# Performance work log

Measured on AMD Instinct MI355X. Metric: run time of the kernel, lower is better.

Reference implementation:

```python
import jax, jax.numpy as jnp
import numpy as np


def setup_inputs() -> dict:
    key = jax.random.key(0)
    k1, k2 = jax.random.split(key)
    z = jax.random.normal(k1, (8, 16, 16, 16, 32), dtype=jnp.float32)
    # codebook initialized uniform(-1/K, 1/K) in the original module
    K = 8192
    emb = jax.random.uniform(k2, (K, 32), dtype=jnp.float32, minval=-1.0 / K, maxval=1.0 / K)
    return {"z": z, "emb": emb}


def reference(z, emb):
    bs, h, w, d, c = z.shape
    z_flat = z.reshape(-1, c)  # [N, c]
    # Squared Euclidean distances: ||z||^2 - 2 z.e + ||e||^2.
    # torch.cdist uses sqrt, but argmin is identical for squared distances
    # and distances are not returned, so we skip the sqrt.
    d2 = (
        jnp.sum(z_flat * z_flat, axis=-1, keepdims=True)
        - 2.0 * (z_flat @ emb.T)
        + jnp.sum(emb * emb, axis=-1)
    )  # [N, K]
    idx = jnp.argmin(d2, axis=1)  # [N]
    quantized = emb[idx].reshape(bs, h, w, d, c)
    commitment_loss = jnp.mean(jnp.square(z - jax.lax.stop_gradient(quantized)))
    vq_loss = jnp.mean(jnp.square(quantized - jax.lax.stop_gradient(z)))
    quantized_st = z + jax.lax.stop_gradient(quantized - z)  # straight-through
    return quantized_st, vq_loss, commitment_loss, idx.reshape(bs, h, w, d)
```

## Files before the change

### kernel.cpp

```cpp
#include <hip/hip_runtime.h>
#include <cfloat>
#include <stdint.h>

#define NROW   32768
#define KCODES 8192
#define CDIM   32
#define OUT_Q    0
#define OUT_LOSS 1048576
#define OUT_IDX  1048578
#define HALF_EPS 1e-4f
#define MAXCAND  32

typedef short bf8_t __attribute__((ext_vector_type(8)));
typedef float f32x4 __attribute__((ext_vector_type(4)));

__device__ __forceinline__ unsigned short f2bf(float f) {
  unsigned int u = __float_as_uint(f);
  return (unsigned short)((u + 0x7FFFu + ((u >> 16) & 1u)) >> 16);
}
__device__ __forceinline__ unsigned int xf(float f) {
  unsigned int u = __float_as_uint(f);
  return u ^ (unsigned int)(((int)u >> 31) | 0x80000000);
}
__device__ __forceinline__ float unxf(unsigned int k) {
  unsigned int u = (k & 0x80000000u) ? (k ^ 0x80000000u) : ~k;
  return __uint_as_float(u);
}

__global__ __launch_bounds__(256) void vq_prep(
    const float* __restrict__ z, const float* __restrict__ emb,
    unsigned short* __restrict__ zh, unsigned short* __restrict__ eh,
    float* __restrict__ enorm, unsigned int* __restrict__ mmax,
    int* __restrict__ ccnt, float* __restrict__ out) {
  const int t = blockIdx.x * 256 + threadIdx.x;
  {
    const float4* z4 = (const float4*)(z + (size_t)t * CDIM);
    unsigned int w[16];
#pragma unroll
    for (int j = 0; j < 8; ++j) {
      float4 v = z4[j];
      w[2 * j]     = (unsigned int)f2bf(v.x) | ((unsigned int)f2bf(v.y) << 16);
      w[2 * j + 1] = (unsigned int)f2bf(v.z) | ((unsigned int)f2bf(v.w) << 16);
    }
    uint4* o = (uint4*)(zh + (size_t)t * CDIM);
#pragma unroll
    for (int j = 0; j < 4; ++j)
      o[j] = make_uint4(w[4 * j], w[4 * j + 1], w[4 * j + 2], w[4 * j + 3]);
  }
  if (t < KCODES) {
    const float4* e4 = (const float4*)(emb + (size_t)t * CDIM);
    float s = 0.f;
    unsigned int w[16];
#pragma unroll
    for (int j = 0; j < 8; ++j) {
      float4 v = e4[j];
      s += v.x * v.x + v.y * v.y + v.z * v.z + v.w * v.w;
      w[2 * j]     = (unsigned int)f2bf(v.x) | ((unsigned int)f2bf(v.y) << 16);
      w[2 * j + 1] = (unsigned int)f2bf(v.z) | ((unsigned int)f2bf(v.w) << 16);
    }
    enorm[t] = s;
    uint4* o = (uint4*)(eh + (size_t)t * CDIM);
#pragma unroll
    for (int j = 0; j < 4; ++j)
      o[j] = make_uint4(w[4 * j], w[4 * j + 1], w[4 * j + 2], w[4 * j + 3]);
  }
  mmax[t] = 0u;
  ccnt[t] = 0;
  if (t < 2) out[OUT_LOSS + t] = 0.f;
}

__global__ __launch_bounds__(256, 4) void vq_sweep_max(
    const unsigned short* __restrict__ zh, const unsigned short* __restrict__ eh,
    unsigned int* __restrict__ mmax) {
  const int wid = threadIdx.x >> 6, lane = threadIdx.x & 63;
  const int quad = lane >> 4, col = lane & 15;
  const int rbase = blockIdx.x * 32;
  const int kbase = wid * 2048;

  bf8_t a0 = *(const bf8_t*)(zh + (size_t)(rbase + col) * CDIM + quad * 8);
  bf8_t a1 = *(const bf8_t*)(zh + (size_t)(rbase + 16 + col) * CDIM + quad * 8);

  float mx0[4], mx1[4];
#pragma unroll
  for (int i = 0; i < 4; ++i) { mx0[i] = -FLT_MAX; mx1[i] = -FLT_MAX; }

  const bf8_t* ep = (const bf8_t*)(eh + ((size_t)kbase + col) * CDIM + quad * 8);
#pragma unroll 4
  for (int t = 0; t < 128; ++t) {
    bf8_t b = ep[(size_t)t * 64];
    f32x4 d0 = __builtin_amdgcn_mfma_f32_16x16x32_bf16(
        a0, b, (f32x4){0.f, 0.f, 0.f, 0.f}, 0, 0, 0);
    f32x4 d1 = __builtin_amdgcn_mfma_f32_16x16x32_bf16(
        a1, b, (f32x4){0.f, 0.f, 0.f, 0.f}, 0, 0, 0);
#pragma unroll
    for (int i = 0; i < 4; ++i) {
      mx0[i] = fmaxf(mx0[i], d0[i]);
      mx1[i] = fmaxf(mx1[i], d1[i]);
    }
  }
#pragma unroll
  for (int off = 1; off < 16; off <<= 1) {
#pragma unroll
    for (int i = 0; i < 4; ++i) {
      mx0[i] = fmaxf(mx0[i], __shfl_xor(mx0[i], off, 64));
      mx1[i] = fmaxf(mx1[i], __shfl_xor(mx1[i], off, 64));
    }
  }
  if (col == 0) {
#pragma unroll
    for (int i = 0; i < 4; ++i) {
      atomicMax(&mmax[rbase + quad * 4 + i], xf(mx0[i]));
      atomicMax(&mmax[rbase + 16 + quad * 4 + i], xf(mx1[i]));
    }
  }
}

__global__ __launch_bounds__(256, 4) void vq_sweep_cand(
    const unsigned short* __restrict__ zh, const unsigned short* __restrict__ eh,
    const unsigned int* __restrict__ mmax, int* __restrict__ ccnt,
    int* __restrict__ cand) {
  const int wid = threadIdx.x >> 6, lane = threadIdx.x & 63;
  const int quad = lane >> 4, col = lane & 15;
  const int rbase = blockIdx.x * 32;
  const int kbase = wid * 2048;

  bf8_t a0 = *(const bf8_t*)(zh + (size_t)(rbase + col) * CDIM + quad * 8);
  bf8_t a1 = *(const bf8_t*)(zh + (size_t)(rbase + 16 + col) * CDIM + quad * 8);

  float th0[4], th1[4];
#pragma unroll
  for (int i = 0; i < 4; ++i) {
    th0[i] = unxf(mmax[rbase + quad * 4 + i]) - HALF_EPS;
    th1[i] = unxf(mmax[rbase + 16 + quad * 4 + i]) - HALF_EPS;
  }

  const bf8_t* ep = (const bf8_t*)(eh + ((size_t)kbase + col) * CDIM + quad * 8);
#pragma unroll 2
  for (int t = 0; t < 128; ++t) {
    bf8_t b = ep[(size_t)t * 64];
    f32x4 d0 = __builtin_amdgcn_mfma_f32_16x16x32_bf16(
        a0, b, (f32x4){0.f, 0.f, 0.f, 0.f}, 0, 0, 0);
    f32x4 d1 = __builtin_amdgcn_mfma_f32_16x16x32_bf16(
        a1, b, (f32x4){0.f, 0.f, 0.f, 0.f}, 0, 0, 0);
    const int code = kbase + t * 16 + col;
#pragma unroll
    for (int i = 0; i < 4; ++i) {
      if (d0[i] >= th0[i]) {
        int r = rbase + quad * 4 + i;
        int s = atomicAdd(&ccnt[r], 1);
        if (s < MAXCAND) cand[(size_t)r * MAXCAND + s] = code;
      }
      if (d1[i] >= th1[i]) {
        int r = rbase + 16 + quad * 4 + i;
        int s = atomicAdd(&ccnt[r], 1);
        if (s < MAXCAND) cand[(size_t)r * MAXCAND + s] = code;
      }
    }
  }
}

__global__ __launch_bounds__(256) void vq_final(
    const float* __restrict__ z, const float* __restrict__ emb,
    const float* __restrict__ enorm, const int* __restrict__ ccnt,
    const int* __restrict__ cand, float* __restrict__ out) {
  const int r = blockIdx.x * 256 + threadIdx.x;

  float zr[CDIM];
  const float4* z4 = (const float4*)(z + (size_t)r * CDIM);
#pragma unroll
  for (int j = 0; j < 8; ++j) {
    float4 v = z4[j];
    zr[4 * j + 0] = v.x; zr[4 * j + 1] = v.y;
    zr[4 * j + 2] = v.z; zr[4 * j + 3] = v.w;
  }
  float znorm = 0.f;
#pragma unroll
  for (int j = 0; j < CDIM; ++j) znorm = fmaf(zr[j], zr[j], znorm);

  const int n = ccnt[r];
  float best = FLT_MAX;
  int bidx = KCODES;
  if (n <= MAXCAND) {
    for (int j = 0; j < n; ++j) {
      int k = cand[(size_t)r * MAXCAND + j];
      const float* ek = emb + (size_t)k * CDIM;
      float dot = 0.f;
#pragma unroll
      for (int q = 0; q < CDIM; ++q) dot = fmaf(zr[q], ek[q], dot);
      float s = fmaf(-2.f, dot, znorm) + enorm[k];
      if (s < best || (s == best && k < bidx)) { best = s; bidx = k; }
    }
  } else {
    for (int k = 0; k < KCODES; ++k) {
      const float* ek = emb + (size_t)k * CDIM;
      float dot = 0.f;
#pragma unroll
      for (int q = 0; q < CDIM; ++q) dot = fmaf(zr[q], ek[q], dot);
      float s = fmaf(-2.f, dot, znorm) + enorm[k];
      if (s < best) { best = s; bidx = k; }
    }
  }

  const float4* q4 = (const float4*)(emb + (size_t)bidx * CDIM);
  float4* o4 = (float4*)(out + OUT_Q + (size_t)r * CDIM);
  float lsum = 0.f;
#pragma unroll
  for (int j = 0; j < 8; ++j) {
    float4 q = q4[j];
    float dx = zr[4 * j + 0] - q.x, dy = zr[4 * j + 1] - q.y;
    float dz = zr[4 * j + 2] - q.z, dw = zr[4 * j + 3] - q.w;
    lsum += dx * dx + dy * dy + dz * dz + dw * dw;
    o4[j] = q;
  }
  out[OUT_IDX + r] = (float)bidx;

#pragma unroll
  for (int off = 32; off > 0; off >>= 1) lsum += __shfl_down(lsum, off, 64);
  if ((threadIdx.x & 63) == 0) {
    float v = lsum * (1.0f / (float)(NROW * CDIM));
    atomicAdd(out + OUT_LOSS + 0, v);
    atomicAdd(out + OUT_LOSS + 1, v);
  }
}

extern "C" void kernel_launch(void* const* d_in, const int* in_sizes, int n_in,
                              void* d_out, int out_size, void* d_ws,
                              size_t ws_size, hipStream_t stream) {
  const float* z = (const float*)d_in[0];
  const float* emb = (const float*)d_in[1];
  float* out = (float*)d_out;

  float* enorm = (float*)d_ws;
  unsigned short* zh = (unsigned short*)(enorm + KCODES);
  unsigned short* eh = zh + (size_t)NROW * CDIM;
  unsigned int* mmax = (unsigned int*)(eh + (size_t)KCODES * CDIM);
  int* ccnt = (int*)(mmax + NROW);
  int* cand = ccnt + NROW;

  vq_prep<<<NROW / 256, 256, 0, stream>>>(z, emb, zh, eh, enorm, mmax, ccnt, out);
  vq_sweep_max<<<NROW / 32, 256, 0, stream>>>(zh, eh, mmax);
  vq_sweep_cand<<<NROW / 32, 256, 0, stream>>>(zh, eh, mmax, ccnt, cand);
  vq_final<<<NROW / 256, 256, 0, stream>>>(z, emb, enorm, ccnt, cand, out);
}
```

Before: 195.6 us.

## Fuse max and candidate sweeps into one block-local kernel with larger row tiles

Merges the two bf16 MFMA sweep kernels into one kernel in which each 512-thread block handles 128 rows across the whole codebook. The per-row max is reduced in shared memory instead of through global atomics, which removes the mmax buffer and one launch. Each B fragment is now reused across 8 row fragments, cutting codebook reloads. A per-tile coarse max test skips most of the per-element threshold checks. Register pressure rises (8 A fragments plus 32 max accumulators), which may limit occupancy, and the prep and final kernels move to 128-thread blocks.

```diff
diff --git a/kernel.cpp b/kernel.cpp
--- a/kernel.cpp
+++ b/kernel.cpp
@@ -27,12 +27,12 @@
   return __uint_as_float(u);
 }
 
-__global__ __launch_bounds__(256) void vq_prep(
+__global__ __launch_bounds__(128) void vq_prep(
     const float* __restrict__ z, const float* __restrict__ emb,
     unsigned short* __restrict__ zh, unsigned short* __restrict__ eh,
-    float* __restrict__ enorm, unsigned int* __restrict__ mmax,
-    int* __restrict__ ccnt, float* __restrict__ out) {
-  const int t = blockIdx.x * 256 + threadIdx.x;
+    float* __restrict__ enorm, int* __restrict__ ccnt,
+    float* __restrict__ out) {
+  const int t = blockIdx.x * 128 + threadIdx.x;
   {
     const float4* z4 = (const float4*)(z + (size_t)t * CDIM);
     unsigned int w[16];
@@ -64,106 +64,122 @@
     for (int j = 0; j < 4; ++j)
       o[j] = make_uint4(w[4 * j], w[4 * j + 1], w[4 * j + 2], w[4 * j + 3]);
   }
-  mmax[t] = 0u;
   ccnt[t] = 0;
   if (t < 2) out[OUT_LOSS + t] = 0.f;
 }
 
-__global__ __launch_bounds__(256, 4) void vq_sweep_max(
+__global__ __launch_bounds__(512, 2) void vq_sweep(
     const unsigned short* __restrict__ zh, const unsigned short* __restrict__ eh,
-    unsigned int* __restrict__ mmax) {
+    int* __restrict__ ccnt, int* __restrict__ cand) {
+  __shared__ unsigned int smax[128][16];
+  __shared__ unsigned int rowmax[128];
   const int wid = threadIdx.x >> 6, lane = threadIdx.x & 63;
   const int quad = lane >> 4, col = lane & 15;
-  const int rbase = blockIdx.x * 32;
-  const int kbase = wid * 2048;
-
-  bf8_t a0 = *(const bf8_t*)(zh + (size_t)(rbase + col) * CDIM + quad * 8);
-  bf8_t a1 = *(const bf8_t*)(zh + (size_t)(rbase + 16 + col) * CDIM + quad * 8);
-
-  float mx0[4], mx1[4];
-#pragma unroll
-  for (int i = 0; i < 4; ++i) { mx0[i] = -FLT_MAX; mx1[i] = -FLT_MAX; }
+  const int rbase = blockIdx.x * 128;
+  const int kbase = wid * 1024;
+
+  for (int i = threadIdx.x; i < 128 * 16; i += 512)
+    ((unsigned int*)smax)[i] = 0u;
+
+  bf8_t a[8];
+#pragma unroll
+  for (int f = 0; f < 8; ++f)
+    a[f] = *(const bf8_t*)(zh + (size_t)(rbase + f * 16 + col) * CDIM + quad * 8);
+
+  float mx[8][4];
+#pragma unroll
+  for (int f = 0; f < 8; ++f)
+#pragma unroll
+    for (int i = 0; i < 4; ++i) mx[f][i] = -FLT_MAX;
 
   const bf8_t* ep = (const bf8_t*)(eh + ((size_t)kbase + col) * CDIM + quad * 8);
-#pragma unroll 4
-  for (int t = 0; t < 128; ++t) {
-    bf8_t b = ep[(size_t)t * 64];
-    f32x4 d0 = __builtin_amdgcn_mfma_f32_16x16x32_bf16(
-        a0, b, (f32x4){0.f, 0.f, 0.f, 0.f}, 0, 0, 0);
-    f32x4 d1 = __builtin_amdgcn_mfma_f32_16x16x32_bf16(
-        a1, b, (f32x4){0.f, 0.f, 0.f, 0.f}, 0, 0, 0);
-#pragma unroll
-    for (int i = 0; i < 4; ++i) {
-      mx0[i] = fmaxf(mx0[i], d0[i]);
-      mx1[i] = fmaxf(mx1[i], d1[i]);
-    }
-  }
-#pragma unroll
-  for (int off = 1; off < 16; off <<= 1) {
-#pragma unroll
-    for (int i = 0; i < 4; ++i) {
-      mx0[i] = fmaxf(mx0[i], __shfl_xor(mx0[i], off, 64));
-      mx1[i] = fmaxf(mx1[i], __shfl_xor(mx1[i], off, 64));
-    }
-  }
-  if (col == 0) {
-#pragma unroll
-    for (int i = 0; i < 4; ++i) {
-      atomicMax(&mmax[rbase + quad * 4 + i], xf(mx0[i]));
-      atomicMax(&mmax[rbase + 16 + quad * 4 + i], xf(mx1[i]));
-    }
-  }
-}
-
-__global__ __launch_bounds__(256, 4) void vq_sweep_cand(
-    const unsigned short* __restrict__ zh, const unsigned short* __restrict__ eh,
-    const unsigned int* __restrict__ mmax, int* __restrict__ ccnt,
-    int* __restrict__ cand) {
-  const int wid = threadIdx.x >> 6, lane = threadIdx.x & 63;
-  const int quad = lane >> 4, col = lane & 15;
-  const int rbase = blockIdx.x * 32;
-  const int kbase = wid * 2048;
-
-  bf8_t a0 = *(const bf8_t*)(zh + (size_t)(rbase + col) * CDIM + quad * 8);
-  bf8_t a1 = *(const bf8_t*)(zh + (size_t)(rbase + 16 + col) * CDIM + quad * 8);
-
-  float th0[4], th1[4];
-#pragma unroll
-  for (int i = 0; i < 4; ++i) {
-    th0[i] = unxf(mmax[rbase + quad * 4 + i]) - HALF_EPS;
-    th1[i] = unxf(mmax[rbase + 16 + quad * 4 + i]) - HALF_EPS;
-  }
-
-  const bf8_t* ep = (const bf8_t*)(eh + ((size_t)kbase + col) * CDIM + quad * 8);
+  const f32x4 zero = {0.f, 0.f, 0.f, 0.f};
+  __syncthreads();
+
 #pragma unroll 2
-  for (int t = 0; t < 128; ++t) {
-    bf8_t b = ep[(size_t)t * 64];
-    f32x4 d0 = __builtin_amdgcn_mfma_f32_16x16x32_bf16(
-        a0, b, (f32x4){0.f, 0.f, 0.f, 0.f}, 0, 0, 0);
-    f32x4 d1 = __builtin_amdgcn_mfma_f32_16x16x32_bf16(
-        a1, b, (f32x4){0.f, 0.f, 0.f, 0.f}, 0, 0, 0);
-    const int code = kbase + t * 16 + col;
-#pragma unroll
-    for (int i = 0; i < 4; ++i) {
-      if (d0[i] >= th0[i]) {
-        int r = rbase + quad * 4 + i;
-        int s = atomicAdd(&ccnt[r], 1);
-        if (s < MAXCAND) cand[(size_t)r * MAXCAND + s] = code;
-      }
-      if (d1[i] >= th1[i]) {
-        int r = rbase + 16 + quad * 4 + i;
-        int s = atomicAdd(&ccnt[r], 1);
-        if (s < MAXCAND) cand[(size_t)r * MAXCAND + s] = code;
-      }
-    }
-  }
-}
-
-__global__ __launch_bounds__(256) void vq_final(
+  for (int tt = 0; tt < 64; tt += 4) {
+    bf8_t b0 = ep[(size_t)(tt + 0) * 64];
+    bf8_t b1 = ep[(size_t)(tt + 1) * 64];
+    bf8_t b2 = ep[(size_t)(tt + 2) * 64];
+    bf8_t b3 = ep[(size_t)(tt + 3) * 64];
+#pragma unroll
+    for (int f = 0; f < 8; ++f) {
+      f32x4 d0 = __builtin_amdgcn_mfma_f32_16x16x32_bf16(a[f], b0, zero, 0, 0, 0);
+      f32x4 d1 = __builtin_amdgcn_mfma_f32_16x16x32_bf16(a[f], b1, zero, 0, 0, 0);
+      f32x4 d2 = __builtin_amdgcn_mfma_f32_16x16x32_bf16(a[f], b2, zero, 0, 0, 0);
+      f32x4 d3 = __builtin_amdgcn_mfma_f32_16x16x32_bf16(a[f], b3, zero, 0, 0, 0);
+#pragma unroll
+      for (int i = 0; i < 4; ++i)
+        mx[f][i] = fmaxf(fmaxf(fmaxf(fmaxf(d0[i], d1[i]), d2[i]), d3[i]), mx[f][i]);
+    }
+  }
+#pragma unroll
+  for (int f = 0; f < 8; ++f)
+#pragma unroll
+    for (int i = 0; i < 4; ++i)
+      atomicMax(&smax[f * 16 + quad * 4 + i][col], xf(mx[f][i]));
+  __syncthreads();
+  if (threadIdx.x < 128) {
+    unsigned int m = 0u;
+#pragma unroll
+    for (int c = 0; c < 16; ++c) {
+      unsigned int v = smax[threadIdx.x][c];
+      if (v > m) m = v;
+    }
+    rowmax[threadIdx.x] = m;
+  }
+  __syncthreads();
+
+  float th[8][4], thmin[8];
+#pragma unroll
+  for (int f = 0; f < 8; ++f) {
+#pragma unroll
+    for (int i = 0; i < 4; ++i)
+      th[f][i] = unxf(rowmax[f * 16 + quad * 4 + i]) - HALF_EPS;
+    thmin[f] = fminf(fminf(th[f][0], th[f][1]), fminf(th[f][2], th[f][3]));
+  }
+
+#define CHECK_TILE(dj, j)                                                    \
+  {                                                                          \
+    float md = fmaxf(fmaxf(dj[0], dj[1]), fmaxf(dj[2], dj[3]));              \
+    if (md >= thmin[f]) {                    \
+      const int code = code0 + (j) * 16;                                     \
+      _Pragma("unroll") for (int i = 0; i < 4; ++i) {                        \
+        if (dj[i] >= th[f][i]) {                                             \
+          int r = rbase + f * 16 + quad * 4 + i;                             \
+          int s = atomicAdd(&ccnt[r], 1);                                    \
+          if (s < MAXCAND) cand[(size_t)r * MAXCAND + s] = code;             \
+        }                                                                    \
+      }                                                                      \
+    }                                                                        \
+  }
+
+  for (int tt = 0; tt < 64; tt += 4) {
+    bf8_t b0 = ep[(size_t)(tt + 0) * 64];
+    bf8_t b1 = ep[(size_t)(tt + 1) * 64];
+    bf8_t b2 = ep[(size_t)(tt + 2) * 64];
+    bf8_t b3 = ep[(size_t)(tt + 3) * 64];
+    const int code0 = kbase + tt * 16 + col;
+#pragma unroll
+    for (int f = 0; f < 8; ++f) {
+      f32x4 d0 = __builtin_amdgcn_mfma_f32_16x16x32_bf16(a[f], b0, zero, 0, 0, 0);
+      f32x4 d1 = __builtin_amdgcn_mfma_f32_16x16x32_bf16(a[f], b1, zero, 0, 0, 0);
+      f32x4 d2 = __builtin_amdgcn_mfma_f32_16x16x32_bf16(a[f], b2, zero, 0, 0, 0);
+      f32x4 d3 = __builtin_amdgcn_mfma_f32_16x16x32_bf16(a[f], b3, zero, 0, 0, 0);
+      CHECK_TILE(d0, 0)
+      CHECK_TILE(d1, 1)
+      CHECK_TILE(d2, 2)
+      CHECK_TILE(d3, 3)
+    }
+  }
+#undef CHECK_TILE
+}
+
+__global__ __launch_bounds__(128) void vq_final(
     const float* __restrict__ z, const float* __restrict__ emb,
     const float* __restrict__ enorm, const int* __restrict__ ccnt,
     const int* __restrict__ cand, float* __restrict__ out) {
-  const int r = blockIdx.x * 256 + threadIdx.x;
+  const int r = blockIdx.x * 128 + threadIdx.x;
 
   float zr[CDIM];
   const float4* z4 = (const float4*)(z + (size_t)r * CDIM);
@@ -233,12 +249,10 @@
   float* enorm = (float*)d_ws;
   unsigned short* zh = (unsigned short*)(enorm + KCODES);
   unsigned short* eh = zh + (size_t)NROW * CDIM;
-  unsigned int* mmax = (unsigned int*)(eh + (size_t)KCODES * CDIM);
-  int* ccnt = (int*)(mmax + NROW);
+  int* ccnt = (int*)(eh + (size_t)KCODES * CDIM);
   int* cand = ccnt + NROW;
 
-  vq_prep<<<NROW / 256, 256, 0, stream>>>(z, emb, zh, eh, enorm, mmax, ccnt, out);
-  vq_sweep_max<<<NROW / 32, 256, 0, stream>>>(zh, eh, mmax);
-  vq_sweep_cand<<<NROW / 32, 256, 0, stream>>>(zh, eh, mmax, ccnt, cand);
-  vq_final<<<NROW / 256, 256, 0, stream>>>(z, emb, enorm, ccnt, cand, out);
-}
+  vq_prep<<<NROW / 128, 128, 0, stream>>>(z, emb, zh, eh, enorm, ccnt, out);
+  vq_sweep<<<NROW / 128, 512, 0, stream>>>(zh, eh, ccnt, cand);
+  vq_final<<<NROW / 128, 128, 0, stream>>>(z, emb, enorm, ccnt, cand, out);
+}
```

Result: faster. 174.4 us (-10.9%).
